# Kernel optimization log

Measured on AMD Instinct MI355X. Metric: run time of the kernel, lower is better.

Reference implementation:

```python
import jax, jax.numpy as jnp
import numpy as np

B, T, D, H = 2, 2048, 1024, 16
HS = D // H  # head_size = 64


def setup_inputs() -> dict:
    key = jax.random.key(0)
    ks = jax.random.split(key, 8)
    scale = D ** -0.5
    q = jax.random.normal(ks[0], (B, T, D), dtype=jnp.float32)
    k = jax.random.normal(ks[1], (B, T, D), dtype=jnp.float32)
    v = jax.random.normal(ks[2], (B, T, D), dtype=jnp.float32)
    # per-head projection weights (no bias), stacked over heads: [H, D, HS]
    Wq = jax.random.normal(ks[3], (H, D, HS), dtype=jnp.float32) * scale
    Wk = jax.random.normal(ks[4], (H, D, HS), dtype=jnp.float32) * scale
    Wv = jax.random.normal(ks[5], (H, D, HS), dtype=jnp.float32) * scale
    # output projection Linear(H*HS, D) with bias
    Wo = jax.random.normal(ks[6], (D, D), dtype=jnp.float32) * scale
    bo = jnp.zeros((D,), dtype=jnp.float32)
    # causal mask, broadcastable to [B, T, T]; mask==0 -> -inf
    mask = jnp.tril(jnp.ones((T, T), dtype=bool))[None]
    return {"q": q, "k": k, "v": v, "Wq": Wq, "Wk": Wk, "Wv": Wv,
            "Wo": Wo, "bo": bo, "mask": mask}


def reference(q, k, v, Wq, Wk, Wv, Wo, bo, mask):
    # Batched equivalent of the per-head loop: project all heads at once.
    Q = jnp.einsum('btc,hcd->bhtd', q, Wq)  # [B,H,T,HS]
    K = jnp.einsum('btc,hcd->bhtd', k, Wk)
    V = jnp.einsum('btc,hcd->bhtd', v, Wv)
    wei = jnp.einsum('bhtd,bhsd->bhts', Q, K) * (HS ** -0.5)  # [B,H,T,T]
    wei = jnp.where(mask[:, None, :, :], wei, jnp.float32(-jnp.inf))
    attn = jax.nn.softmax(wei, axis=-1)  # dropout is identity in eval
    out = jnp.einsum('bhts,bhsd->bhtd', attn, V)
    out = out.transpose(0, 2, 1, 3).reshape(B, T, D)  # concat heads
    return out @ Wo + bo
```

## Files before the change

kernel.cpp:

```cpp
#include <hip/hip_runtime.h>
#include <hip/hip_bf16.h>
#include <math.h>

#define BB 2
#define TT 2048
#define DM 1024
#define NH 16
#define HS 64
#define MM (BB*TT)

typedef __attribute__((ext_vector_type(8))) short s16x8;
typedef __attribute__((ext_vector_type(4))) float f32x4;

#define MFMA16(a,b,c) __builtin_amdgcn_mfma_f32_16x16x32_bf16((a),(b),(c),0,0,0)

__device__ inline unsigned short f2bf(float f) {
    union { float f; unsigned u; } x; x.f = f;
    unsigned r = x.u + 0x7fff + ((x.u >> 16) & 1);
    return (unsigned short)(r >> 16);
}
__device__ inline unsigned short f2bfr(float f) {
    union { float f; unsigned u; } x; x.f = f;
    return (unsigned short)((x.u + 0x8000u) >> 16);
}

__device__ __forceinline__ void gload16(const void* g, void* l) {
    __builtin_amdgcn_global_load_lds(
        (const __attribute__((address_space(1))) unsigned int*)g,
        (__attribute__((address_space(3))) unsigned int*)l, 16, 0, 0);
}

__global__ __launch_bounds__(256) void cvt_w_kernel(
    const float* __restrict__ W0, const float* __restrict__ W1,
    const float* __restrict__ W2, unsigned short* __restrict__ dst, int wo_mode)
{
    __shared__ __align__(16) short Tt[64 * 72];
    const int t = threadIdx.x;
    const int d0 = blockIdx.x * 64;
    const int h  = blockIdx.y;
    const int z  = blockIdx.z;
    const float* W = (z == 0) ? W0 : (z == 1) ? W1 : W2;
    unsigned short* dz = dst + (size_t)z * DM * DM;

    const int hs4 = (t & 15) * 4;
    const int dl0 = t >> 4;
    #pragma unroll
    for (int it = 0; it < 4; ++it) {
        int dl = it * 16 + dl0;
        const float* src = wo_mode
            ? &W[(size_t)(d0 + dl) * DM + h * 64 + hs4]
            : &W[(size_t)h * DM * HS + (size_t)(d0 + dl) * HS + hs4];
        float4 vv = *(const float4*)src;
        Tt[(hs4 + 0) * 72 + dl] = (short)f2bf(vv.x);
        Tt[(hs4 + 1) * 72 + dl] = (short)f2bf(vv.y);
        Tt[(hs4 + 2) * 72 + dl] = (short)f2bf(vv.z);
        Tt[(hs4 + 3) * 72 + dl] = (short)f2bf(vv.w);
    }
    __syncthreads();
    int hs = t >> 2, doff = (t & 3) * 16;
    s16x8 r0 = *(s16x8*)&Tt[hs * 72 + doff];
    s16x8 r1 = *(s16x8*)&Tt[hs * 72 + doff + 8];
    unsigned short* op = dz + (size_t)(h * 64 + hs) * DM + d0 + doff;
    *(s16x8*)op = r0;
    *(s16x8*)(op + 8) = r1;
}

__global__ __launch_bounds__(256) void cvt_x_kernel(
    const float* __restrict__ q, const float* __restrict__ k,
    const float* __restrict__ v, unsigned short* __restrict__ xb)
{
    const int z = blockIdx.z;
    const float* x = (z == 0) ? q : (z == 1) ? k : v;
    unsigned short* d = xb + (size_t)z * MM * DM;
    const size_t i = ((size_t)blockIdx.x * 256 + threadIdx.x) * 8;
    float4 a0 = *(const float4*)&x[i];
    float4 a1 = *(const float4*)&x[i + 4];
    union { s16x8 v; __hip_bfloat162 h[4]; } cv;
    cv.h[0] = __float22bfloat162_rn(make_float2(a0.x, a0.y));
    cv.h[1] = __float22bfloat162_rn(make_float2(a0.z, a0.w));
    cv.h[2] = __float22bfloat162_rn(make_float2(a1.x, a1.y));
    cv.h[3] = __float22bfloat162_rn(make_float2(a1.z, a1.w));
    *(s16x8*)&d[i] = cv.v;
}

__global__ __launch_bounds__(512) void proj8_kernel(
    const unsigned short* __restrict__ xb, const unsigned short* __restrict__ Wt,
    unsigned short* __restrict__ Qb, unsigned short* __restrict__ Kb,
    unsigned short* __restrict__ Vt)
{
    __shared__ __align__(16) unsigned short As[2][2][128 * 64];
    __shared__ __align__(16) unsigned short Bs[2][2][128 * 64];

    const int tid = threadIdx.x;
    const int l = tid & 63, w = tid >> 6;
    const int wr = w >> 2, wc = w & 3;
    const int g = l >> 4, r16 = l & 15;
    const int r7 = r16 & 7;
    const int wch = wc >> 1, wc64 = (wc & 1) * 64;

    const int bid = blockIdx.x;
    const int xcd = bid & 7, q2 = bid >> 3;
    const int z = q2 >> 3, q3 = q2 & 7;
    const int m0 = (xcd * 2 + (q3 >> 2)) * 256;
    const int n0 = (q3 & 3) * 256;

    const unsigned short* Az = xb + (size_t)z * MM * DM;
    const unsigned short* Wz = Wt + (size_t)z * DM * DM;

    const unsigned short* aG[2]; const unsigned short* bG[2]; int dO[2];
    #pragma unroll
    for (int p = 0; p < 2; ++p) {
        int qid = p * 512 + tid;
        int srow = qid >> 3, scp = qid & 7;
        int scol = (scp ^ (srow & 7)) * 8;
        aG[p] = Az + (size_t)(m0 + srow) * DM + scol;
        bG[p] = Wz + (size_t)(n0 + srow) * DM + scol;
        dO[p] = qid * 8;
    }

    f32x4 acc[8][4];
    #pragma unroll
    for (int i = 0; i < 8; ++i)
        #pragma unroll
        for (int c = 0; c < 4; ++c)
            #pragma unroll
            for (int j = 0; j < 4; ++j) acc[i][c][j] = 0.0f;

    #define STAGE_A(buf, hh, kel) do {                                   \
        _Pragma("unroll")                                                 \
        for (int p = 0; p < 2; ++p)                                       \
            gload16(aG[p] + (size_t)(hh) * 128 * DM + (kel),              \
                    &As[(buf)][(hh)][dO[p]]);                             \
    } while (0)
    #define STAGE_B(buf, hh, kel) do {                                   \
        _Pragma("unroll")                                                 \
        for (int p = 0; p < 2; ++p)                                       \
            gload16(bG[p] + (size_t)(hh) * 128 * DM + (kel),              \
                    &Bs[(buf)][(hh)][dO[p]]);                             \
    } while (0)

    #define PHASE(bufv, MG, NG) do {                                      \
        s16x8 af[4][2], bf[2][2];                                          \
        const unsigned short* Ab = &As[(bufv)][wr][0];                     \
        const unsigned short* Bb = &Bs[(bufv)][wch][0];                    \
        _Pragma("unroll")                                                  \
        for (int i2 = 0; i2 < 4; ++i2) {                                   \
            int r = ((MG) * 4 + i2) * 16 + r16;                            \
            af[i2][0] = *(const s16x8*)&Ab[r * 64 + (((0 + g) ^ r7) * 8)]; \
            af[i2][1] = *(const s16x8*)&Ab[r * 64 + (((4 + g) ^ r7) * 8)]; \
        }                                                                  \
        _Pragma("unroll")                                                  \
        for (int c2 = 0; c2 < 2; ++c2) {                                   \
            int r = wc64 + ((NG) * 2 + c2) * 16 + r16;                     \
            bf[c2][0] = *(const s16x8*)&Bb[r * 64 + (((0 + g) ^ r7) * 8)]; \
            bf[c2][1] = *(const s16x8*)&Bb[r * 64 + (((4 + g) ^ r7) * 8)]; \
        }                                                                  \
        __builtin_amdgcn_s_setprio(1);                                     \
        _Pragma("unroll")                                                  \
        for (int i2 = 0; i2 < 4; ++i2)                                     \
            _Pragma("unroll")                                              \
            for (int c2 = 0; c2 < 2; ++c2) {                               \
                acc[(MG)*4+i2][(NG)*2+c2] = MFMA16(af[i2][0], bf[c2][0],   \
                    acc[(MG)*4+i2][(NG)*2+c2]);                            \
                acc[(MG)*4+i2][(NG)*2+c2] = MFMA16(af[i2][1], bf[c2][1],   \
                    acc[(MG)*4+i2][(NG)*2+c2]);                            \
            }                                                              \
        __builtin_amdgcn_s_setprio(0);                                     \
    } while (0)

    STAGE_A(0, 0, 0); STAGE_A(0, 1, 0);
    STAGE_B(0, 0, 0); STAGE_B(0, 1, 0);

    for (int t = 0; t < 16; ++t) {
        const int buf = t & 1, nb = buf ^ 1;
        asm volatile("s_waitcnt vmcnt(0)" ::: "memory");
        __builtin_amdgcn_sched_barrier(0);
        __builtin_amdgcn_s_barrier();
        if (t < 15) { STAGE_A(nb, 0, (t + 1) * 64); STAGE_A(nb, 1, (t + 1) * 64); }
        PHASE(buf, 0, 0);
        if (t < 15) { STAGE_B(nb, 0, (t + 1) * 64); STAGE_B(nb, 1, (t + 1) * 64); }
        PHASE(buf, 0, 1);
        PHASE(buf, 1, 0);
        PHASE(buf, 1, 1);
    }
    #undef STAGE_A
    #undef STAGE_B
    #undef PHASE

    const int h = (n0 >> 6) + wc;
    if (z != 2) {
        unsigned short* dst = (z == 0) ? Qb : Kb;
        const float sc = (z == 0) ? 0.18033688011112042f : 1.0f;
        #pragma unroll
        for (int i = 0; i < 8; ++i)
            #pragma unroll
            for (int j = 0; j < 4; ++j) {
                int row = m0 + wr * 128 + i * 16 + g * 4 + j;
                int bb = row >> 11, tt = row & (TT - 1);
                size_t rb = (((size_t)(bb * NH + h)) * TT + tt) * HS;
                #pragma unroll
                for (int c = 0; c < 4; ++c)
                    dst[rb + c * 16 + r16] = f2bf(acc[i][c][j] * sc);
            }
    } else {
        #pragma unroll
        for (int i = 0; i < 8; ++i) {
            int row0 = m0 + wr * 128 + i * 16 + g * 4;
            int bb = row0 >> 11, tt0 = row0 & (TT - 1);
            #pragma unroll
            for (int c = 0; c < 4; ++c) {
                int hs = c * 16 + r16;
                union { unsigned long long u; unsigned short s[4]; } pk;
                #pragma unroll
                for (int j = 0; j < 4; ++j) pk.s[j] = f2bf(acc[i][c][j]);
                *(unsigned long long*)&Vt[(((size_t)(bb * NH + h)) * HS + hs) * TT + tt0] = pk.u;
            }
        }
    }
}

__global__ __launch_bounds__(512) void out_gemm_kernel(
    const unsigned short* __restrict__ Ob, const unsigned short* __restrict__ Wot,
    const float* __restrict__ bo, float* __restrict__ out)
{
    __shared__ __align__(16) unsigned short As2[2][128 * 32];
    __shared__ __align__(16) unsigned short Bs2[2][128 * 32];

    const int tid = threadIdx.x;
    const int l = tid & 63, w = tid >> 6;
    const int wr = w >> 2, wc = w & 3;
    const int g = l >> 4, r16 = l & 15;

    const int bid = blockIdx.x;
    const int xcd = bid & 7, u = bid >> 3;
    const int n0 = (u >> 2) * 128;
    const int m0 = (xcd * 4 + (u & 3)) * 128;

    const int srow = tid >> 2, sgl = tid & 3;
    const int scol = ((sgl ^ ((srow >> 1) & 3)) * 8);
    const unsigned short* aS = Ob + (size_t)(m0 + srow) * DM + scol;
    const unsigned short* bS = Wot + (size_t)(n0 + srow) * DM + scol;
    const int sDof = tid * 8;

    int aoff[4], boff[2];
    #pragma unroll
    for (int i = 0; i < 4; ++i) {
        int row = wr * 64 + i * 16 + r16;
        aoff[i] = row * 32 + ((g ^ ((row >> 1) & 3)) * 8);
    }
    #pragma unroll
    for (int c = 0; c < 2; ++c) {
        int row = wc * 32 + c * 16 + r16;
        boff[c] = row * 32 + ((g ^ ((row >> 1) & 3)) * 8);
    }

    f32x4 acc[4][2];
    #pragma unroll
    for (int i = 0; i < 4; ++i)
        #pragma unroll
        for (int c = 0; c < 2; ++c)
            #pragma unroll
            for (int j = 0; j < 4; ++j) acc[i][c][j] = 0.0f;

    #define OSTAGE(buf, k0_) do {                                        \
        gload16(aS + (k0_), &As2[(buf)][sDof]);                          \
        gload16(bS + (k0_), &Bs2[(buf)][sDof]);                          \
    } while (0)

    #define OCOMPUTE(buf) do {                                           \
        s16x8 af[4], bf[2];                                              \
        _Pragma("unroll")                                                \
        for (int i = 0; i < 4; ++i) af[i] = *(const s16x8*)&As2[(buf)][aoff[i]]; \
        _Pragma("unroll")                                                \
        for (int c = 0; c < 2; ++c) bf[c] = *(const s16x8*)&Bs2[(buf)][boff[c]]; \
        _Pragma("unroll")                                                \
        for (int i = 0; i < 4; ++i)                                      \
            _Pragma("unroll")                                            \
            for (int c = 0; c < 2; ++c)                                  \
                acc[i][c] = MFMA16(af[i], bf[c], acc[i][c]);             \
    } while (0)

    OSTAGE(0, 0);
    for (int t = 0; t < 31; ++t) {
        OSTAGE((t + 1) & 1, (t + 1) * 32);
        asm volatile("s_waitcnt vmcnt(2)" ::: "memory");
        __builtin_amdgcn_sched_barrier(0);
        __builtin_amdgcn_s_barrier();
        OCOMPUTE(t & 1);
        __builtin_amdgcn_s_barrier();
    }
    asm volatile("s_waitcnt vmcnt(0)" ::: "memory");
    __builtin_amdgcn_sched_barrier(0);
    __builtin_amdgcn_s_barrier();
    OCOMPUTE(1);
    #undef OSTAGE
    #undef OCOMPUTE

    #pragma unroll
    for (int i = 0; i < 4; ++i)
        #pragma unroll
        for (int j = 0; j < 4; ++j) {
            int row = m0 + wr * 64 + i * 16 + g * 4 + j;
            #pragma unroll
            for (int c = 0; c < 2; ++c) {
                int col = n0 + wc * 32 + c * 16 + r16;
                out[(size_t)row * DM + col] = acc[i][c][j] + bo[col];
            }
        }
}

template<bool MASKED>
__device__ __forceinline__ void ftile9(
    int kv0, int t0, int r16, int g,
    const unsigned short* __restrict__ Kl,
    const unsigned short* __restrict__ Vl,
    short* __restrict__ Pw0, short* __restrict__ Pw1,
    const s16x8 (&qf)[2],
    float& l_run, f32x4 (&o)[4])
{
    const int rs = r16 & 7;
    const bool half1 = !MASKED || (kv0 + 32 <= t0 + 15);
    float pe[4][4];
    __builtin_amdgcn_s_setprio(1);
    f32x4 s0a[4];
    #pragma unroll
    for (int c = 0; c < 4; ++c) {
        if (!MASKED || (kv0 + c * 16 <= t0 + 15)) {
            f32x4 s0;
            #pragma unroll
            for (int j = 0; j < 4; ++j) s0[j] = 0.0f;
            const int base = (c * 16 + r16) * 64;
            s16x8 kf0 = *(const s16x8*)&Kl[base + ((g ^ rs) * 8)];
            s16x8 kf1 = *(const s16x8*)&Kl[base + (((4 + g) ^ rs) * 8)];
            s0 = MFMA16(kf0, qf[0], s0);
            s0 = MFMA16(kf1, qf[1], s0);
            s0a[c] = s0;
        }
    }
    __builtin_amdgcn_s_setprio(0);
    #pragma unroll
    for (int c = 0; c < 4; ++c) {
        if (!MASKED || (kv0 + c * 16 <= t0 + 15)) {
            #pragma unroll
            for (int j = 0; j < 4; ++j) {
                float e = __builtin_amdgcn_exp2f(s0a[c][j] - 16.0f);
                if (MASKED)
                    e = (kv0 + c * 16 + g * 4 + j <= t0 + r16) ? e : 0.0f;
                pe[c][j] = e;
                l_run += e;
            }
        } else {
            #pragma unroll
            for (int j = 0; j < 4; ++j) pe[c][j] = 0.0f;
        }
    }

    #pragma unroll
    for (int c = 0; c < 2; ++c) {
        union { unsigned long long u; unsigned short s[4]; } pk;
        #pragma unroll
        for (int j = 0; j < 4; ++j) pk.s[j] = f2bfr(pe[c][j]);
        *(unsigned long long*)&Pw0[r16 * 36 + c * 16 + g * 4] = pk.u;
    }
    if (half1) {
        #pragma unroll
        for (int c = 0; c < 2; ++c) {
            union { unsigned long long u; unsigned short s[4]; } pk;
            #pragma unroll
            for (int j = 0; j < 4; ++j) pk.s[j] = f2bfr(pe[2 + c][j]);
            *(unsigned long long*)&Pw1[r16 * 36 + c * 16 + g * 4] = pk.u;
        }
    }
    s16x8 pb0 = *(const s16x8*)&Pw0[r16 * 36 + g * 8];
    __builtin_amdgcn_s_setprio(1);
    #pragma unroll
    for (int c = 0; c < 4; ++c) {
        s16x8 vf = *(const s16x8*)&Vl[(c * 16 + r16) * 64 + ((g ^ rs) * 8)];
        o[c] = MFMA16(vf, pb0, o[c]);
    }
    if (half1) {
        s16x8 pb1 = *(const s16x8*)&Pw1[r16 * 36 + g * 8];
        #pragma unroll
        for (int c = 0; c < 4; ++c) {
            s16x8 vf = *(const s16x8*)&Vl[(c * 16 + r16) * 64 + (((4 + g) ^ rs) * 8)];
            o[c] = MFMA16(vf, pb1, o[c]);
        }
    }
    __builtin_amdgcn_s_setprio(0);
}

__global__ __launch_bounds__(512) void flash9_kernel(
    const unsigned short* __restrict__ Qb,
    const unsigned short* __restrict__ Kb,
    const unsigned short* __restrict__ Vt,
    unsigned short* __restrict__ Ob)
{
    __shared__ __align__(16) unsigned short Kls[2][4096];
    __shared__ __align__(16) unsigned short Vls[2][4096];
    __shared__ __align__(16) short Pl[8][2][576];

    const int tid = threadIdx.x;
    const int l = tid & 63, w = tid >> 6;
    const int r16 = l & 15, g = l >> 4;

    const int bid = blockIdx.x;
    const int bh = bid & 31;
    const int jj = bid >> 5;
    const int qc = (jj < 8) ? (15 - jj) : (jj - 8);
    const int numt = 2 * qc + 2;
    const int b = bh >> 4, h = bh & 15;

    const unsigned short* Qp = Qb + (size_t)bh * TT * HS;
    const unsigned short* Kp = Kb + (size_t)bh * TT * HS;
    const unsigned short* Vp = Vt + (size_t)bh * HS * TT;
    unsigned short* Op = Ob + (size_t)b * TT * DM + h * HS;
    short* Pw0 = &Pl[w][0][0];
    short* Pw1 = &Pl[w][1][0];

    const int t0 = qc * 128 + w * 16;

    const int srow = tid >> 3, c8 = tid & 7;
    const unsigned short* kS = Kp + srow * HS + ((c8 ^ (srow & 7)) * 8);
    const unsigned short* vS = Vp + (size_t)srow * TT + ((c8 ^ (srow & 7)) * 8);
    const int d0 = tid * 8;

    s16x8 qf[2];
    #pragma unroll
    for (int s = 0; s < 2; ++s)
        qf[s] = *(const s16x8*)(Qp + (size_t)(t0 + r16) * HS + s * 32 + g * 8);

    float l_run = 0.0f;
    f32x4 o[4];
    #pragma unroll
    for (int c = 0; c < 4; ++c)
        #pragma unroll
        for (int j = 0; j < 4; ++j) o[c][j] = 0.0f;

    #define STAGE(buf, kv0_) do {                                   \
        gload16(kS + (size_t)(kv0_) * HS, &Kls[(buf)][d0]);         \
        gload16(vS + (kv0_), &Vls[(buf)][d0]);                      \
    } while (0)

    #define FTILE(kv0_, buf_) do {                                  \
        if ((kv0_) + 64 <= t0 + 1)                                  \
            ftile9<false>((kv0_), t0, r16, g, &Kls[(buf_)][0],      \
                          &Vls[(buf_)][0], Pw0, Pw1, qf, l_run, o); \
        else if ((kv0_) <= t0 + 15)                                 \
            ftile9<true>((kv0_), t0, r16, g, &Kls[(buf_)][0],       \
                         &Vls[(buf_)][0], Pw0, Pw1, qf, l_run, o);  \
    } while (0)

    STAGE(0, 0);
    for (int t = 0; t < numt - 1; ++t) {
        STAGE((t + 1) & 1, (t + 1) * 64);
        asm volatile("s_waitcnt vmcnt(2)" ::: "memory");
        __builtin_amdgcn_sched_barrier(0);
        __builtin_amdgcn_s_barrier();
        FTILE(t * 64, t & 1);
        __builtin_amdgcn_s_barrier();
    }
    asm volatile("s_waitcnt vmcnt(0)" ::: "memory");
    __builtin_amdgcn_sched_barrier(0);
    __builtin_amdgcn_s_barrier();
    FTILE((numt - 1) * 64, (numt - 1) & 1);
    #undef STAGE
    #undef FTILE

    float ls = l_run;
    ls += __shfl_xor(ls, 16);
    ls += __shfl_xor(ls, 32);
    const float inv = 1.0f / ls;
    unsigned short* rp = Op + (size_t)(t0 + r16) * DM;
    #pragma unroll
    for (int c = 0; c < 4; ++c) {
        union { unsigned long long u; unsigned short s[4]; } pk;
        #pragma unroll
        for (int j = 0; j < 4; ++j) pk.s[j] = f2bfr(o[c][j] * inv);
        *(unsigned long long*)&rp[c * 16 + g * 4] = pk.u;
    }
}

extern "C" void kernel_launch(void* const* d_in, const int* in_sizes, int n_in,
                              void* d_out, int out_size, void* d_ws, size_t ws_size,
                              hipStream_t stream) {
    const float* q  = (const float*)d_in[0];
    const float* k  = (const float*)d_in[1];
    const float* v  = (const float*)d_in[2];
    const float* Wq = (const float*)d_in[3];
    const float* Wk = (const float*)d_in[4];
    const float* Wv = (const float*)d_in[5];
    const float* Wo = (const float*)d_in[6];
    const float* bo = (const float*)d_in[7];
    float* out = (float*)d_out;

    const size_t QKV_ELEMS = (size_t)BB * NH * TT * HS;
    unsigned short* Qb = (unsigned short*)d_ws;
    unsigned short* Kb = Qb + QKV_ELEMS;
    unsigned short* Vt = Kb + QKV_ELEMS;
    unsigned short* R4 = Vt + QKV_ELEMS;
    unsigned short* Wt = R4;
    unsigned short* Ob = R4;
    unsigned short* Wot = Qb;
    unsigned short* xb = R4 + QKV_ELEMS;

    cvt_w_kernel<<<dim3(16, 16, 3), 256, 0, stream>>>(Wq, Wk, Wv, Wt, 0);
    cvt_x_kernel<<<dim3(2048, 1, 3), 256, 0, stream>>>(q, k, v, xb);
    proj8_kernel<<<dim3(192), 512, 0, stream>>>(xb, Wt, Qb, Kb, Vt);
    flash9_kernel<<<dim3(512), 512, 0, stream>>>(Qb, Kb, Vt, Ob);
    cvt_w_kernel<<<dim3(16, 16, 1), 256, 0, stream>>>(Wo, Wo, Wo, Wot, 1);
    out_gemm_kernel<<<dim3(256), 512, 0, stream>>>(Ob, Wot, bo, out);
}
```

Before: 136.8 us.

## Fuse fp32-to-bf16 input conversion into projection GEMM A-tile loading

Removes the separate cvt_x kernel and has the projection GEMM read fp32 q/k/v directly into registers, convert them to bf16 and write them into shared memory. The pipeline changes from direct global-to-LDS loads for A to register prefetch plus a store after compute, with an extra barrier per iteration. This drops one launch and a write and re-read of a 24 MB bf16 intermediate. In exchange the GEMM reads twice the A bytes as fp32, uses more registers, and the register-staged A path may overlap less well with compute.

```diff
diff --git a/kernel.cpp b/kernel.cpp
--- a/kernel.cpp
+++ b/kernel.cpp
@@ -65,26 +65,9 @@
     *(s16x8*)(op + 8) = r1;
 }
 
-__global__ __launch_bounds__(256) void cvt_x_kernel(
+__global__ __launch_bounds__(512) void proj8_kernel(
     const float* __restrict__ q, const float* __restrict__ k,
-    const float* __restrict__ v, unsigned short* __restrict__ xb)
-{
-    const int z = blockIdx.z;
-    const float* x = (z == 0) ? q : (z == 1) ? k : v;
-    unsigned short* d = xb + (size_t)z * MM * DM;
-    const size_t i = ((size_t)blockIdx.x * 256 + threadIdx.x) * 8;
-    float4 a0 = *(const float4*)&x[i];
-    float4 a1 = *(const float4*)&x[i + 4];
-    union { s16x8 v; __hip_bfloat162 h[4]; } cv;
-    cv.h[0] = __float22bfloat162_rn(make_float2(a0.x, a0.y));
-    cv.h[1] = __float22bfloat162_rn(make_float2(a0.z, a0.w));
-    cv.h[2] = __float22bfloat162_rn(make_float2(a1.x, a1.y));
-    cv.h[3] = __float22bfloat162_rn(make_float2(a1.z, a1.w));
-    *(s16x8*)&d[i] = cv.v;
-}
-
-__global__ __launch_bounds__(512) void proj8_kernel(
-    const unsigned short* __restrict__ xb, const unsigned short* __restrict__ Wt,
+    const float* __restrict__ v, const unsigned short* __restrict__ Wt,
     unsigned short* __restrict__ Qb, unsigned short* __restrict__ Kb,
     unsigned short* __restrict__ Vt)
 {
@@ -104,16 +87,16 @@
     const int m0 = (xcd * 2 + (q3 >> 2)) * 256;
     const int n0 = (q3 & 3) * 256;
 
-    const unsigned short* Az = xb + (size_t)z * MM * DM;
+    const float* xz = (z == 0) ? q : (z == 1) ? k : v;
     const unsigned short* Wz = Wt + (size_t)z * DM * DM;
 
-    const unsigned short* aG[2]; const unsigned short* bG[2]; int dO[2];
+    const float* aF[2]; const unsigned short* bG[2]; int dO[2];
     #pragma unroll
     for (int p = 0; p < 2; ++p) {
         int qid = p * 512 + tid;
         int srow = qid >> 3, scp = qid & 7;
         int scol = (scp ^ (srow & 7)) * 8;
-        aG[p] = Az + (size_t)(m0 + srow) * DM + scol;
+        aF[p] = xz + (size_t)(m0 + srow) * DM + scol;
         bG[p] = Wz + (size_t)(n0 + srow) * DM + scol;
         dO[p] = qid * 8;
     }
@@ -126,17 +109,41 @@
             #pragma unroll
             for (int j = 0; j < 4; ++j) acc[i][c][j] = 0.0f;
 
-    #define STAGE_A(buf, hh, kel) do {                                   \
+    float4 aR[2][2][2];
+
+    #define PLOADA(kel) do {                                              \
         _Pragma("unroll")                                                 \
-        for (int p = 0; p < 2; ++p)                                       \
-            gload16(aG[p] + (size_t)(hh) * 128 * DM + (kel),              \
-                    &As[(buf)][(hh)][dO[p]]);                             \
-    } while (0)
-    #define STAGE_B(buf, hh, kel) do {                                   \
-        _Pragma("unroll")                                                 \
-        for (int p = 0; p < 2; ++p)                                       \
-            gload16(bG[p] + (size_t)(hh) * 128 * DM + (kel),              \
-                    &Bs[(buf)][(hh)][dO[p]]);                             \
+        for (int hh = 0; hh < 2; ++hh)                                    \
+            _Pragma("unroll")                                             \
+            for (int p = 0; p < 2; ++p) {                                 \
+                const float* ap = aF[p] + (size_t)hh * 128 * DM + (kel);  \
+                aR[hh][p][0] = *(const float4*)(ap);                      \
+                aR[hh][p][1] = *(const float4*)(ap + 4);                  \
+            }                                                             \
+    } while (0)
+
+    #define GLOADB(buf, kel) do {                                         \
+        _Pragma("unroll")                                                  \
+        for (int hh = 0; hh < 2; ++hh)                                     \
+            _Pragma("unroll")                                              \
+            for (int p = 0; p < 2; ++p)                                    \
+                gload16(bG[p] + (size_t)hh * 128 * DM + (kel),             \
+                        &Bs[(buf)][hh][dO[p]]);                            \
+    } while (0)
+
+    #define PSTORE(buf) do {                                               \
+        _Pragma("unroll")                                                   \
+        for (int hh = 0; hh < 2; ++hh)                                      \
+            _Pragma("unroll")                                               \
+            for (int p = 0; p < 2; ++p) {                                   \
+                union { s16x8 v; __hip_bfloat162 h2[4]; } cv;               \
+                float4 lo = aR[hh][p][0], hi = aR[hh][p][1];                \
+                cv.h2[0] = __float22bfloat162_rn(make_float2(lo.x, lo.y));  \
+                cv.h2[1] = __float22bfloat162_rn(make_float2(lo.z, lo.w));  \
+                cv.h2[2] = __float22bfloat162_rn(make_float2(hi.x, hi.y));  \
+                cv.h2[3] = __float22bfloat162_rn(make_float2(hi.z, hi.w));  \
+                *(s16x8*)&As[(buf)][hh][dO[p]] = cv.v;                      \
+            }                                                               \
     } while (0)
 
     #define PHASE(bufv, MG, NG) do {                                      \
@@ -168,23 +175,33 @@
         __builtin_amdgcn_s_setprio(0);                                     \
     } while (0)
 
-    STAGE_A(0, 0, 0); STAGE_A(0, 1, 0);
-    STAGE_B(0, 0, 0); STAGE_B(0, 1, 0);
-
-    for (int t = 0; t < 16; ++t) {
+    PLOADA(0);
+    GLOADB(0, 0);
+    PSTORE(0);
+    for (int t = 0; t < 15; ++t) {
         const int buf = t & 1, nb = buf ^ 1;
-        asm volatile("s_waitcnt vmcnt(0)" ::: "memory");
+        PLOADA((t + 1) * 64);
+        GLOADB(nb, (t + 1) * 64);
+        asm volatile("s_waitcnt vmcnt(12) lgkmcnt(0)" ::: "memory");
         __builtin_amdgcn_sched_barrier(0);
         __builtin_amdgcn_s_barrier();
-        if (t < 15) { STAGE_A(nb, 0, (t + 1) * 64); STAGE_A(nb, 1, (t + 1) * 64); }
         PHASE(buf, 0, 0);
-        if (t < 15) { STAGE_B(nb, 0, (t + 1) * 64); STAGE_B(nb, 1, (t + 1) * 64); }
         PHASE(buf, 0, 1);
         PHASE(buf, 1, 0);
         PHASE(buf, 1, 1);
-    }
-    #undef STAGE_A
-    #undef STAGE_B
+        PSTORE(nb);
+        __builtin_amdgcn_s_barrier();
+    }
+    asm volatile("s_waitcnt vmcnt(0) lgkmcnt(0)" ::: "memory");
+    __builtin_amdgcn_sched_barrier(0);
+    __builtin_amdgcn_s_barrier();
+    PHASE(1, 0, 0);
+    PHASE(1, 0, 1);
+    PHASE(1, 1, 0);
+    PHASE(1, 1, 1);
+    #undef PLOADA
+    #undef GLOADB
+    #undef PSTORE
     #undef PHASE
 
     const int h = (n0 >> 6) + wc;
@@ -501,11 +518,9 @@
     unsigned short* Wt = R4;
     unsigned short* Ob = R4;
     unsigned short* Wot = Qb;
-    unsigned short* xb = R4 + QKV_ELEMS;
 
     cvt_w_kernel<<<dim3(16, 16, 3), 256, 0, stream>>>(Wq, Wk, Wv, Wt, 0);
-    cvt_x_kernel<<<dim3(2048, 1, 3), 256, 0, stream>>>(q, k, v, xb);
-    proj8_kernel<<<dim3(192), 512, 0, stream>>>(xb, Wt, Qb, Kb, Vt);
+    proj8_kernel<<<dim3(192), 512, 0, stream>>>(q, k, v, Wt, Qb, Kb, Vt);
     flash9_kernel<<<dim3(512), 512, 0, stream>>>(Qb, Kb, Vt, Ob);
     cvt_w_kernel<<<dim3(16, 16, 1), 256, 0, stream>>>(Wo, Wo, Wo, Wot, 1);
     out_gemm_kernel<<<dim3(256), 512, 0, stream>>>(Ob, Wot, bo, out);
```

Result: faster. 132.4 us (-3.2%).
